# Kernel optimization log

Measured on AMD Instinct MI355X. Metric: run time of the kernel, lower is better.

The kernel has to match this reference:

```python
import jax, jax.numpy as jnp
import numpy as np

M = 8192        # number of variables (len(z), R is MxM)
MAX_K = 256     # max active components (self.max_k)
THRESH = 0.01   # gamma threshold used to drop topk entries


def setup_inputs() -> dict:
    key = jax.random.key(0)
    ks = jax.random.split(key, 6)
    # R is an LD-correlation-like PSD matrix (required for logdet / inverse)
    A = jax.random.normal(ks[0], (M, M), dtype=jnp.float32)
    R = A @ A.T / M + 0.1 * jnp.eye(M, dtype=jnp.float32)
    z = jax.random.normal(ks[1], (M,), dtype=jnp.float32)
    sigma2 = jax.random.uniform(ks[2], (M,), jnp.float32, 0.05, 1.0)
    p = jax.random.uniform(ks[3], (M,), jnp.float32, 0.01, 0.99)
    pq = jax.random.uniform(ks[4], (M,), jnp.float32, 0.01, 0.99)
    gamma = jax.random.uniform(ks[5], (M,), jnp.float32, 1e-4, 1.0)
    # S = inv(R) @ z, computed once in the module __init__ (a constant buffer)
    S = jnp.linalg.inv(R) @ z
    N = 100000  # GWAS sample size (python int scalar)
    return {"R": R, "z": z, "sigma2": sigma2, "p": p, "pq": pq,
            "gamma": gamma, "S": S, "N": N}


def reference(R, z, sigma2, p, pq, gamma, S, N):
    # topk + threshold filter, expressed with a fixed-size mask (jit-friendly).
    u, ind = jax.lax.top_k(gamma, MAX_K)                  # [MAX_K]
    mask = (u > THRESH).astype(R.dtype)                   # 1 for kept indices
    # U = N * diag(sigma2*gamma)[:, ind] is column-sparse: column j has single
    # nonzero vals[j] at row ind[j]. Masked columns are exactly zero, which
    # makes sigma identity in those columns, so logdet/inverse reduce to the
    # active kxk block -- identical math to the dynamic-k torch version.
    vals = N * sigma2[ind] * gamma[ind] * mask            # [MAX_K]
    Rk = R[ind]                                           # V = R[ind, :], [MAX_K, M]
    Rkk = Rk[:, ind]                                      # [MAX_K, MAX_K]
    # sigma = I_k + V @ U  (V@U collapses to Rkk scaled per-column by vals)
    sigma = jnp.eye(MAX_K, dtype=R.dtype) + Rkk * vals[None, :]
    inv = jnp.linalg.inv(sigma)
    logdet = jnp.linalg.slogdet(sigma)[1]                 # sigma is PD
    # quadratic_form = -z^T (I - U inv V) S / 2, without materializing MxM
    zU = z[ind] * vals                                    # z^T U, [MAX_K]
    VS = Rk @ S                                           # V S,   [MAX_K]
    quadratic_form = -(z @ S - zU @ (inv @ VS)) / 2
    log_likelihood = -logdet / 2 + quadratic_form
    # Bernoulli KL over the active set
    x2 = pq[ind]
    x1 = p[ind]
    kl = jnp.sum(mask * (x2 * (jnp.log(x2) - jnp.log(x1))
                         + (1 - x2) * (jnp.log(1 - x2) - jnp.log(1 - x1))))
    return -log_likelihood + kl
```

## Files before the change

### kernel.cpp

```cpp
#include <hip/hip_runtime.h>
#include <cstdint>
#include <cstddef>


#define BLK_STRIDE 68
#define PK_TOTAL (528 * BLK_STRIDE)

typedef __attribute__((ext_vector_type(8))) short short8_t;
typedef __attribute__((ext_vector_type(16))) float f32x16;

__device__ __forceinline__ int blk_off(int I, int J) {
  return (((I * (I + 1)) >> 1) + J) * BLK_STRIDE;
}

__device__ __forceinline__ float bcast_lane(float v, int lane) {
  return __int_as_float(__builtin_amdgcn_readlane(__float_as_int(v), lane));
}

__device__ __forceinline__ void split_bf16(float f, short& h, short& l) {
  unsigned u = __float_as_uint(f);
  unsigned hr = (u + 0x7FFFu + ((u >> 16) & 1u)) >> 16;
  h = (short)hr;
  float hf = __uint_as_float(hr << 16);
  float lf = f - hf;
  unsigned u2 = __float_as_uint(lf);
  l = (short)((u2 + 0x7FFFu + ((u2 >> 16) & 1u)) >> 16);
}

__global__ __launch_bounds__(256) void k_topk(
    const float* __restrict__ gamma, const float* __restrict__ sigma2,
    const float* __restrict__ z, const float* __restrict__ p,
    const float* __restrict__ pq, const int* __restrict__ Nptr,
    int* __restrict__ ind, float* __restrict__ sqv,
    float* __restrict__ t1, float* __restrict__ klt) {
  __shared__ __align__(16) float g[8 * 1032];
  int t = threadIdx.x;
  const float4* ga4 = (const float4*)gamma;
  #pragma unroll
  for (int m = 0; m < 8; ++m) {
    int i = 4 * (t + m * 256);
    float4 v = ga4[t + m * 256];
    *(float4*)&g[i + 8 * (i >> 10)] = v;
  }
  __syncthreads();
  int e = blockIdx.x * 32 + (t >> 3);
  int chunk = t & 7;
  float ge = g[e + 8 * (e >> 10)];
  const float4* g4 = (const float4*)g;
  int i4base = chunk * 258;
  int jbase = chunk * 1024;
  int cnt = 0;
  for (int it = 0; it < 256; ++it) {
    float4 v = g4[i4base + it];
    int j = jbase + 4 * it;
    cnt += (v.x > ge || (v.x == ge && (j + 0) < e)) ? 1 : 0;
    cnt += (v.y > ge || (v.y == ge && (j + 1) < e)) ? 1 : 0;
    cnt += (v.z > ge || (v.z == ge && (j + 2) < e)) ? 1 : 0;
    cnt += (v.w > ge || (v.w == ge && (j + 3) < e)) ? 1 : 0;
  }
  cnt += __shfl_xor(cnt, 1);
  cnt += __shfl_xor(cnt, 2);
  cnt += __shfl_xor(cnt, 4);
  if (chunk == 0 && cnt < 256) {
    float u = ge;
    float mask = (u > 0.01f) ? 1.0f : 0.0f;
    float fN = (float)Nptr[0];
    float vals = fN * sigma2[e] * u * mask;
    float sq = sqrtf(vals);
    ind[cnt] = e;
    sqv[cnt] = sq;
    t1[cnt] = sq * z[e];
    float x1 = p[e], x2 = pq[e];
    klt[cnt] = mask * (x2 * (logf(x2) - logf(x1)) +
                       (1.0f - x2) * (logf(1.0f - x2) - logf(1.0f - x1)));
  }
}

__global__ __launch_bounds__(256) void k_vs(
    const float* __restrict__ R, const float* __restrict__ S,
    const float* __restrict__ z, const int* __restrict__ ind,
    const float* __restrict__ sqv, float* __restrict__ Mp_g,
    float* __restrict__ t2, float* __restrict__ zS) {
  __shared__ __align__(16) float row[8192];
  __shared__ float red[4];
  int t = threadIdx.x;
  int b = blockIdx.x;
  if (b < 256) {
    int ridx = ind[b];
    const float4* Rr = (const float4*)(R + (size_t)ridx * 8192);
    const float4* S4 = (const float4*)S;
    float4* row4 = (float4*)row;
    float acc = 0.0f;
    #pragma unroll
    for (int m = 0; m < 8; ++m) {
      float4 v = Rr[t + m * 256];
      row4[t + m * 256] = v;
      float4 s = S4[t + m * 256];
      acc += v.x * s.x + v.y * s.y + v.z * s.z + v.w * s.w;
    }
    #pragma unroll
    for (int o = 32; o > 0; o >>= 1) acc += __shfl_down(acc, o);
    if ((t & 63) == 0) red[t >> 6] = acc;
    __syncthreads();
    float svb = sqv[b];
    if (t == 0) t2[b] = svb * (red[0] + red[1] + red[2] + red[3]);
    if ((t >> 3) <= (b >> 3)) {
      int cj = ind[t];
      float rv = row[cj];
      Mp_g[blk_off(b >> 3, t >> 3) + (b & 7) * 8 + (t & 7)] =
          svb * sqv[t] * rv + ((t == b) ? 1.0f : 0.0f);
    }
  } else {
    const float4* z4 = (const float4*)z;
    const float4* S4 = (const float4*)S;
    float acc = 0.0f;
    #pragma unroll
    for (int m = 0; m < 8; ++m) {
      float4 a = z4[t + m * 256];
      float4 s = S4[t + m * 256];
      acc += a.x * s.x + a.y * s.y + a.z * s.z + a.w * s.w;
    }
    #pragma unroll
    for (int o = 32; o > 0; o >>= 1) acc += __shfl_down(acc, o);
    if ((t & 63) == 0) red[t >> 6] = acc;
    __syncthreads();
    if (t == 0) zS[0] = red[0] + red[1] + red[2] + red[3];
  }
}

__global__ __launch_bounds__(256, 1) void k_chol(
    const float* __restrict__ Mp_g, const float* __restrict__ t1w,
    const float* __restrict__ t2w, const float* __restrict__ kltw,
    const float* __restrict__ zSw, float* __restrict__ out) {
  __shared__ __align__(16) float Mp[PK_TOTAL];
  __shared__ __align__(16) float Ld[32 * 36];
  __shared__ float rhs1[256], rhs2[256], dv[256];
  __shared__ float idv32[32], y1[32], y2[32];
  __shared__ float red[12];
  int t = threadIdx.x;

  {
    const float4* src = (const float4*)Mp_g;
    float4* dst = (float4*)Mp;
    for (int i = t; i < PK_TOTAL / 4; i += 256) dst[i] = src[i];
  }
  rhs1[t] = t1w[t];
  rhs2[t] = t2w[t];
  __syncthreads();

  for (int K = 0; K < 8; ++K) {
    int base = K * 32;
    int nb = 224 - base;
    if (t < 64) {
      if (t < 32) {
        int r = t;
        int I = (base >> 3) + (r >> 3);
        float a[32];
        #pragma unroll
        for (int cb = 0; cb < 4; ++cb) {
          float4 v0 = {0.f, 0.f, 0.f, 0.f}, v1 = {0.f, 0.f, 0.f, 0.f};
          if (cb <= (r >> 3)) {
            int o = blk_off(I, (base >> 3) + cb) + (r & 7) * 8;
            v0 = *(const float4*)&Mp[o];
            v1 = *(const float4*)&Mp[o + 4];
          }
          a[cb * 8 + 0] = v0.x; a[cb * 8 + 1] = v0.y;
          a[cb * 8 + 2] = v0.z; a[cb * 8 + 3] = v0.w;
          a[cb * 8 + 4] = v1.x; a[cb * 8 + 5] = v1.y;
          a[cb * 8 + 6] = v1.z; a[cb * 8 + 7] = v1.w;
        }
        float myrt = 1.0f, myrinv = 1.0f;
        #pragma unroll
        for (int k = 0; k < 32; ++k) {
          float d = bcast_lane(a[k], k);
          float rinv = rsqrtf(d);
          float rt = d * rinv;
          float m = (r == k) ? rt : a[k] * rinv;
          if (r == k) { myrt = rt; myrinv = rinv; }
          a[k] = m;
          #pragma unroll
          for (int c = k + 1; c < 32; ++c) {
            float lck = bcast_lane(m, c);
            if (r >= c) a[c] -= m * lck;
          }
        }
        #pragma unroll
        for (int c = 0; c < 32; ++c) Ld[r * 36 + c] = a[c];
        dv[base + r] = myrt;
        idv32[r] = myrinv;
      }
      __builtin_amdgcn_wave_barrier();
      asm volatile("s_waitcnt lgkmcnt(0)" ::: "memory");
      __builtin_amdgcn_sched_barrier(0);
      {
        int r = t & 31;
        float v = (t < 32) ? rhs1[base + r] : rhs2[base + r];
        #pragma unroll
        for (int k = 0; k < 32; ++k) {
          float vk = __shfl(v, (t & 32) | k, 64);
          float yk = vk * idv32[k];
          if (r == k) v = yk;
          else if (r > k) v -= Ld[r * 36 + k] * yk;
        }
        if (t < 32) { rhs1[base + r] = v; y1[r] = v; }
        else        { rhs2[base + r] = v; y2[r] = v; }
      }
    }
    __syncthreads();
    if (nb > 0 && t < nb) {
      int gi = base + 32 + t;
      int I = gi >> 3, Jb = base >> 3;
      float a[32];
      #pragma unroll
      for (int cb = 0; cb < 4; ++cb) {
        int o = blk_off(I, Jb + cb) + (gi & 7) * 8;
        float4 v0 = *(const float4*)&Mp[o];
        float4 v1 = *(const float4*)&Mp[o + 4];
        a[cb * 8 + 0] = v0.x; a[cb * 8 + 1] = v0.y;
        a[cb * 8 + 2] = v0.z; a[cb * 8 + 3] = v0.w;
        a[cb * 8 + 4] = v1.x; a[cb * 8 + 5] = v1.y;
        a[cb * 8 + 6] = v1.z; a[cb * 8 + 7] = v1.w;
      }
      #pragma unroll
      for (int c = 0; c < 32; ++c) {
        float s = a[c];
        #pragma unroll
        for (int k = 0; k < c; ++k) s -= a[k] * Ld[c * 36 + k];
        a[c] = s * idv32[c];
      }
      float s1 = 0.0f, s2 = 0.0f;
      #pragma unroll
      for (int k = 0; k < 32; ++k) { s1 += a[k] * y1[k]; s2 += a[k] * y2[k]; }
      rhs1[gi] -= s1;
      rhs2[gi] -= s2;
      #pragma unroll
      for (int cb = 0; cb < 4; ++cb) {
        int o = blk_off(I, Jb + cb) + (gi & 7) * 8;
        short8_t h8, l8;
        #pragma unroll
        for (int e = 0; e < 8; ++e) {
          short hh, ll;
          split_bf16(a[cb * 8 + e], hh, ll);
          h8[e] = hh;
          l8[e] = ll;
        }
        *(short8_t*)&Mp[o] = h8;
        *(short8_t*)&Mp[o + 4] = l8;
      }
    }
    __syncthreads();
    if (nb > 0) {
      int nbb = nb >> 5;
      int ntiles = (nbb * (nbb + 1)) >> 1;
      int w = t >> 6, ln = t & 63;
      int lane31 = ln & 31, kh = ln >> 5;
      for (int idx = w; idx < ntiles; idx += 4) {
        int ti = 0;
        while ((((ti + 1) * (ti + 2)) >> 1) <= idx) ++ti;
        int tj = idx - ((ti * (ti + 1)) >> 1);
        int r_abs = base + 32 + ti * 32 + lane31;
        int c_abs = base + 32 + tj * 32 + lane31;
        f32x16 acc = {};
        #pragma unroll
        for (int k0 = 0; k0 < 2; ++k0) {
          int kb = base + k0 * 16 + kh * 8;
          int oa = blk_off(r_abs >> 3, kb >> 3) + (r_abs & 7) * 8;
          int ob = blk_off(c_abs >> 3, kb >> 3) + (c_abs & 7) * 8;
          short8_t ahi = *(const short8_t*)&Mp[oa];
          short8_t alo = *(const short8_t*)&Mp[oa + 4];
          short8_t bhi = *(const short8_t*)&Mp[ob];
          short8_t blo = *(const short8_t*)&Mp[ob + 4];
          acc = __builtin_amdgcn_mfma_f32_32x32x16_bf16(ahi, bhi, acc, 0, 0, 0);
          acc = __builtin_amdgcn_mfma_f32_32x32x16_bf16(ahi, blo, acc, 0, 0, 0);
          acc = __builtin_amdgcn_mfma_f32_32x32x16_bf16(alo, bhi, acc, 0, 0, 0);
        }
        int Rb = base + 32 + ti * 32;
        int Cc = base + 32 + tj * 32 + lane31;
        #pragma unroll
        for (int reg = 0; reg < 16; ++reg) {
          int Rr = Rb + (reg & 3) + 8 * (reg >> 2) + 4 * kh;
          if ((Cc >> 3) <= (Rr >> 3)) {
            int o = blk_off(Rr >> 3, Cc >> 3) + (Rr & 7) * 8 + (Cc & 7);
            Mp[o] -= acc[reg];
          }
        }
      }
    }
    __syncthreads();
  }

  float v1 = logf(dv[t]);
  float v2 = rhs1[t] * rhs2[t];
  float v3 = kltw[t];
  #pragma unroll
  for (int o = 32; o > 0; o >>= 1) {
    v1 += __shfl_down(v1, o);
    v2 += __shfl_down(v2, o);
    v3 += __shfl_down(v3, o);
  }
  if ((t & 63) == 0) {
    int w = t >> 6;
    red[w] = v1; red[4 + w] = v2; red[8 + w] = v3;
  }
  __syncthreads();
  if (t == 0) {
    float ld = 0.0f, q = 0.0f, kl = 0.0f;
    for (int w = 0; w < 4; ++w) {
      ld += red[w]; q += red[4 + w]; kl += red[8 + w];
    }
    out[0] = ld + 0.5f * (zSw[0] - q) + kl;
  }
}

extern "C" void kernel_launch(void* const* d_in, const int* in_sizes, int n_in,
                              void* d_out, int out_size, void* d_ws, size_t ws_size,
                              hipStream_t stream) {
  const float* R      = (const float*)d_in[0];
  const float* z      = (const float*)d_in[1];
  const float* sigma2 = (const float*)d_in[2];
  const float* p      = (const float*)d_in[3];
  const float* pq     = (const float*)d_in[4];
  const float* gamma  = (const float*)d_in[5];
  const float* S      = (const float*)d_in[6];
  const int*   Nptr   = (const int*)d_in[7];
  float* out = (float*)d_out;

  float* wsf  = (float*)d_ws;
  float* Mp_g = wsf;
  int*   ind  = (int*)(wsf + PK_TOTAL);
  float* sqv  = wsf + PK_TOTAL + 256;
  float* t1   = wsf + PK_TOTAL + 512;
  float* t2   = wsf + PK_TOTAL + 768;
  float* klt  = wsf + PK_TOTAL + 1024;
  float* zS   = wsf + PK_TOTAL + 1280;

  k_topk<<<256, 256, 0, stream>>>(gamma, sigma2, z, p, pq, Nptr,
                                  ind, sqv, t1, klt);
  k_vs<<<257, 256, 0, stream>>>(R, S, z, ind, sqv, Mp_g, t2, zS);
  k_chol<<<1, 256, 0, stream>>>(Mp_g, t1, t2, klt, zS, out);
}
```

Measured before the change: 165.1 us.

## Shrink Cholesky panel width from 32 to 16 in blocked factorization

Halves the panel width of the blocked Cholesky (16 panels of 16 columns instead of 8 of 32). This shortens the serial single-wave diagonal factorization and the per-row triangular solves, which likely dominate the critical path. In exchange it doubles the number of panel iterations and block barriers. The trailing update still uses 32-aligned MFMA tiles, so it now needs extra masking and can do redundant work on partial tiles.

```diff
diff --git a/kernel.cpp b/kernel.cpp
--- a/kernel.cpp
+++ b/kernel.cpp
@@ -133,9 +133,9 @@
     const float* __restrict__ t2w, const float* __restrict__ kltw,
     const float* __restrict__ zSw, float* __restrict__ out) {
   __shared__ __align__(16) float Mp[PK_TOTAL];
-  __shared__ __align__(16) float Ld[32 * 36];
+  __shared__ __align__(16) float Ld[16 * 17];
   __shared__ float rhs1[256], rhs2[256], dv[256];
-  __shared__ float idv32[32], y1[32], y2[32];
+  __shared__ float idv16[16], y1[16], y2[16];
   __shared__ float red[12];
   int t = threadIdx.x;
 
@@ -148,19 +148,21 @@
   rhs2[t] = t2w[t];
   __syncthreads();
 
-  for (int K = 0; K < 8; ++K) {
-    int base = K * 32;
-    int nb = 224 - base;
-    if (t < 64) {
-      if (t < 32) {
+  #pragma unroll 1
+  for (int K = 0; K < 16; ++K) {
+    int base = K * 16;
+    int Jb = base >> 3;
+    int pstart = base + 16;
+    if (t < 32) {
+      if (t < 16) {
         int r = t;
-        int I = (base >> 3) + (r >> 3);
-        float a[32];
-        #pragma unroll
-        for (int cb = 0; cb < 4; ++cb) {
+        int I = Jb + (r >> 3);
+        float a[16];
+        #pragma unroll
+        for (int cb = 0; cb < 2; ++cb) {
           float4 v0 = {0.f, 0.f, 0.f, 0.f}, v1 = {0.f, 0.f, 0.f, 0.f};
           if (cb <= (r >> 3)) {
-            int o = blk_off(I, (base >> 3) + cb) + (r & 7) * 8;
+            int o = blk_off(I, Jb + cb) + (r & 7) * 8;
             v0 = *(const float4*)&Mp[o];
             v1 = *(const float4*)&Mp[o + 4];
           }
@@ -171,7 +173,7 @@
         }
         float myrt = 1.0f, myrinv = 1.0f;
         #pragma unroll
-        for (int k = 0; k < 32; ++k) {
+        for (int k = 0; k < 16; ++k) {
           float d = bcast_lane(a[k], k);
           float rinv = rsqrtf(d);
           float rt = d * rinv;
@@ -179,40 +181,41 @@
           if (r == k) { myrt = rt; myrinv = rinv; }
           a[k] = m;
           #pragma unroll
-          for (int c = k + 1; c < 32; ++c) {
+          for (int c = k + 1; c < 16; ++c) {
             float lck = bcast_lane(m, c);
             if (r >= c) a[c] -= m * lck;
           }
         }
         #pragma unroll
-        for (int c = 0; c < 32; ++c) Ld[r * 36 + c] = a[c];
+        for (int c = 0; c < 16; ++c) Ld[r * 17 + c] = a[c];
         dv[base + r] = myrt;
-        idv32[r] = myrinv;
+        idv16[r] = myrinv;
       }
       __builtin_amdgcn_wave_barrier();
       asm volatile("s_waitcnt lgkmcnt(0)" ::: "memory");
       __builtin_amdgcn_sched_barrier(0);
       {
-        int r = t & 31;
-        float v = (t < 32) ? rhs1[base + r] : rhs2[base + r];
-        #pragma unroll
-        for (int k = 0; k < 32; ++k) {
-          float vk = __shfl(v, (t & 32) | k, 64);
-          float yk = vk * idv32[k];
+        int r = t & 15;
+        float v = (t < 16) ? rhs1[base + r] : rhs2[base + r];
+        #pragma unroll
+        for (int k = 0; k < 16; ++k) {
+          float vk = __shfl(v, (t & 16) | k, 64);
+          float yk = vk * idv16[k];
           if (r == k) v = yk;
-          else if (r > k) v -= Ld[r * 36 + k] * yk;
-        }
-        if (t < 32) { rhs1[base + r] = v; y1[r] = v; }
+          else if (r > k) v -= Ld[r * 17 + k] * yk;
+        }
+        if (t < 16) { rhs1[base + r] = v; y1[r] = v; }
         else        { rhs2[base + r] = v; y2[r] = v; }
       }
     }
     __syncthreads();
+    int nb = 256 - pstart;
     if (nb > 0 && t < nb) {
-      int gi = base + 32 + t;
-      int I = gi >> 3, Jb = base >> 3;
-      float a[32];
+      int gi = pstart + t;
+      int I = gi >> 3;
+      float a[16];
       #pragma unroll
-      for (int cb = 0; cb < 4; ++cb) {
+      for (int cb = 0; cb < 2; ++cb) {
         int o = blk_off(I, Jb + cb) + (gi & 7) * 8;
         float4 v0 = *(const float4*)&Mp[o];
         float4 v1 = *(const float4*)&Mp[o + 4];
@@ -222,19 +225,19 @@
         a[cb * 8 + 6] = v1.z; a[cb * 8 + 7] = v1.w;
       }
       #pragma unroll
-      for (int c = 0; c < 32; ++c) {
+      for (int c = 0; c < 16; ++c) {
         float s = a[c];
         #pragma unroll
-        for (int k = 0; k < c; ++k) s -= a[k] * Ld[c * 36 + k];
-        a[c] = s * idv32[c];
+        for (int k = 0; k < c; ++k) s -= a[k] * Ld[c * 17 + k];
+        a[c] = s * idv16[c];
       }
       float s1 = 0.0f, s2 = 0.0f;
       #pragma unroll
-      for (int k = 0; k < 32; ++k) { s1 += a[k] * y1[k]; s2 += a[k] * y2[k]; }
+      for (int k = 0; k < 16; ++k) { s1 += a[k] * y1[k]; s2 += a[k] * y2[k]; }
       rhs1[gi] -= s1;
       rhs2[gi] -= s2;
       #pragma unroll
-      for (int cb = 0; cb < 4; ++cb) {
+      for (int cb = 0; cb < 2; ++cb) {
         int o = blk_off(I, Jb + cb) + (gi & 7) * 8;
         short8_t h8, l8;
         #pragma unroll
@@ -250,36 +253,34 @@
     }
     __syncthreads();
     if (nb > 0) {
-      int nbb = nb >> 5;
+      int tb0 = pstart >> 5;
+      int nbb = 8 - tb0;
       int ntiles = (nbb * (nbb + 1)) >> 1;
       int w = t >> 6, ln = t & 63;
       int lane31 = ln & 31, kh = ln >> 5;
+      int Jk = Jb + kh;
       for (int idx = w; idx < ntiles; idx += 4) {
         int ti = 0;
         while ((((ti + 1) * (ti + 2)) >> 1) <= idx) ++ti;
         int tj = idx - ((ti * (ti + 1)) >> 1);
-        int r_abs = base + 32 + ti * 32 + lane31;
-        int c_abs = base + 32 + tj * 32 + lane31;
+        int r_abs = (tb0 + ti) * 32 + lane31;
+        int c_abs = (tb0 + tj) * 32 + lane31;
+        int oa = blk_off(r_abs >> 3, Jk) + (r_abs & 7) * 8;
+        int ob = blk_off(c_abs >> 3, Jk) + (c_abs & 7) * 8;
+        short8_t ahi = *(const short8_t*)&Mp[oa];
+        short8_t alo = *(const short8_t*)&Mp[oa + 4];
+        short8_t bhi = *(const short8_t*)&Mp[ob];
+        short8_t blo = *(const short8_t*)&Mp[ob + 4];
         f32x16 acc = {};
-        #pragma unroll
-        for (int k0 = 0; k0 < 2; ++k0) {
-          int kb = base + k0 * 16 + kh * 8;
-          int oa = blk_off(r_abs >> 3, kb >> 3) + (r_abs & 7) * 8;
-          int ob = blk_off(c_abs >> 3, kb >> 3) + (c_abs & 7) * 8;
-          short8_t ahi = *(const short8_t*)&Mp[oa];
-          short8_t alo = *(const short8_t*)&Mp[oa + 4];
-          short8_t bhi = *(const short8_t*)&Mp[ob];
-          short8_t blo = *(const short8_t*)&Mp[ob + 4];
-          acc = __builtin_amdgcn_mfma_f32_32x32x16_bf16(ahi, bhi, acc, 0, 0, 0);
-          acc = __builtin_amdgcn_mfma_f32_32x32x16_bf16(ahi, blo, acc, 0, 0, 0);
-          acc = __builtin_amdgcn_mfma_f32_32x32x16_bf16(alo, bhi, acc, 0, 0, 0);
-        }
-        int Rb = base + 32 + ti * 32;
-        int Cc = base + 32 + tj * 32 + lane31;
+        acc = __builtin_amdgcn_mfma_f32_32x32x16_bf16(ahi, bhi, acc, 0, 0, 0);
+        acc = __builtin_amdgcn_mfma_f32_32x32x16_bf16(ahi, blo, acc, 0, 0, 0);
+        acc = __builtin_amdgcn_mfma_f32_32x32x16_bf16(alo, bhi, acc, 0, 0, 0);
+        int Rb = (tb0 + ti) * 32;
+        int Cc = c_abs;
         #pragma unroll
         for (int reg = 0; reg < 16; ++reg) {
           int Rr = Rb + (reg & 3) + 8 * (reg >> 2) + 4 * kh;
-          if ((Cc >> 3) <= (Rr >> 3)) {
+          if (Rr >= pstart && Cc >= pstart && (Cc >> 3) <= (Rr >> 3)) {
             int o = blk_off(Rr >> 3, Cc >> 3) + (Rr & 7) * 8 + (Cc & 7);
             Mp[o] -= acc[reg];
           }
```

Measured after the change: 198.7 us. 1.2x slower.
